# Optimization experiments

Measured on AMD Instinct MI355X. Metric: run time of the kernel, lower is better.

Reference implementation:

```python
import jax, jax.numpy as jnp
import numpy as np

NEG = -1e30


def setup_inputs() -> dict:
    key = jax.random.key(0)
    ks = jax.random.split(key, 8)
    B, d, Lc, Lq = 32, 128, 2048, 512
    C = jax.random.normal(ks[0], (B, d, Lc), dtype=jnp.float32)
    Q = jax.random.normal(ks[1], (B, d, Lq), dtype=jnp.float32)
    Cmask = jax.random.randint(ks[2], (B, Lc), 0, 2, dtype=jnp.int32)
    Qmask = jax.random.randint(ks[3], (B, Lq), 0, 2, dtype=jnp.int32)
    # xavier_uniform over (d, 1): bound = sqrt(6 / (d + 1))
    bnd = float(np.sqrt(6.0 / (d + 1)))
    w_c = jax.random.uniform(ks[4], (d, 1), minval=-bnd, maxval=bnd, dtype=jnp.float32)
    w_q = jax.random.uniform(ks[5], (d, 1), minval=-bnd, maxval=bnd, dtype=jnp.float32)
    bnd_m = float(np.sqrt(6.0 / (1 + d)))
    w_mul = jax.random.uniform(ks[6], (1, 1, d), minval=-bnd_m, maxval=bnd_m, dtype=jnp.float32)
    bias = jnp.zeros((1,), dtype=jnp.float32)
    return {"C": C, "Q": Q, "Cmask": Cmask, "Qmask": Qmask,
            "w_c": w_c, "w_q": w_q, "w_mul": w_mul, "bias": bias}


def reference(C, Q, Cmask, Qmask, w_c, w_q, w_mul, bias):
    # C: [B, d, Lc], Q: [B, d, Lq] -> transpose to token-major
    Ct = jnp.swapaxes(C, 1, 2)  # [B, Lc, d]
    Qt = jnp.swapaxes(Q, 1, 2)  # [B, Lq, d]
    cm = Cmask.astype(jnp.float32)[:, :, None]   # [B, Lc, 1]
    qm = Qmask.astype(jnp.float32)[:, None, :]   # [B, 1, Lq]
    # optimized trilinear similarity S: [B, Lc, Lq] (dropout p=0 / eval mode)
    s0 = Ct @ w_c                                  # [B, Lc, 1]
    s1 = jnp.swapaxes(Qt @ w_q, 1, 2)              # [B, 1, Lq]
    s2 = jnp.einsum('bcd,bqd->bcq', Ct * w_mul, Qt)  # [B, Lc, Lq]
    S = s0 + s1 + s2 + bias
    S1 = jax.nn.softmax(S + NEG * (1.0 - qm), axis=2)  # mask over query axis
    S2 = jax.nn.softmax(S + NEG * (1.0 - cm), axis=1)  # mask over context axis
    A = jnp.einsum('bcq,bqd->bcd', S1, Qt)             # [B, Lc, d]
    Bm = jnp.einsum('bck,bkd->bcd', jnp.einsum('bcq,bkq->bck', S1, S2), Ct)
    out = jnp.concatenate([Ct, A, Ct * A, Ct * Bm], axis=2)  # [B, Lc, 4d]
    return jnp.swapaxes(out, 1, 2)  # [B, 4d, Lc]
```

## Files before the change

kernel.cpp:

```cpp
#include <hip/hip_runtime.h>

#define B_ 32
#define D_ 128
#define LC 2048
#define LQ 512
#define CCH 16

#define NEGINF (-3.0e38f)

typedef __attribute__((ext_vector_type(8))) short bf16x8;
typedef __attribute__((ext_vector_type(4))) float f32x4;
typedef __attribute__((ext_vector_type(8))) unsigned short us8;
typedef __attribute__((ext_vector_type(8))) _Float16 f16x8;

__device__ __forceinline__ unsigned short bf16rne(float x) {
    unsigned int u = __float_as_uint(x);
    u = (u + 0x7FFFu + ((u >> 16) & 1u)) >> 16;
    return (unsigned short)u;
}

__device__ __forceinline__ void gll16(const void* g, void* l) {
    __builtin_amdgcn_global_load_lds((const __attribute__((address_space(1))) void*)g,
                                     (__attribute__((address_space(3))) void*)l, 16, 0, 0);
}

__global__ void k_dotw(const float* __restrict__ X, const float* __restrict__ w,
                       float* __restrict__ outv, int L) {
    int idx = blockIdx.x * 256 + threadIdx.x;
    int b = idx / L, x = idx - b * L;
    const float* Xp = X + (size_t)b * D_ * L + x;
    float acc = 0.f;
#pragma unroll 8
    for (int dd = 0; dd < D_; ++dd) acc += Xp[(size_t)dd * L] * w[dd];
    outv[idx] = acc;
}

__global__ void k_prep_C(const float* __restrict__ C, const float* __restrict__ wmul,
                         short* __restrict__ Ctw, short* __restrict__ Cb16) {
    int b = blockIdx.y, c0 = blockIdx.x * 64;
    __shared__ float Tf[128][65];
    __shared__ float wm[128];
    int t = threadIdx.x;
    if (t < 128) wm[t] = wmul[t];
    const float* Cb = C + (size_t)b * D_ * LC;
#pragma unroll
    for (int i = 0; i < 8; ++i) {
        int idx = t + i * 256;
        int d = idx >> 4, c4 = idx & 15;
        float4 v = *(const float4*)(Cb + (size_t)d * LC + c0 + c4 * 4);
        Tf[d][c4 * 4 + 0] = v.x; Tf[d][c4 * 4 + 1] = v.y;
        Tf[d][c4 * 4 + 2] = v.z; Tf[d][c4 * 4 + 3] = v.w;
        ushort4 cv;
        cv.x = bf16rne(v.x); cv.y = bf16rne(v.y); cv.z = bf16rne(v.z); cv.w = bf16rne(v.w);
        *(ushort4*)(Cb16 + ((size_t)b * D_ + d) * LC + c0 + c4 * 4) = cv;
    }
    __syncthreads();
    int c_l = t & 63, g = t >> 6;
    unsigned short u[32];
#pragma unroll
    for (int j = 0; j < 32; ++j) {
        int d = g * 32 + j;
        u[j] = bf16rne(Tf[d][c_l] * wm[d]);
    }
    short* dst = Ctw + ((size_t)b * LC + c0 + c_l) * D_ + g * 32;
#pragma unroll
    for (int k = 0; k < 4; ++k) *(us8*)(dst + k * 8) = *(const us8*)&u[k * 8];
}

__global__ void k_prep_Q(const float* __restrict__ Q, short* __restrict__ Qt16,
                         short* __restrict__ Wf) {
    int b = blockIdx.y, q0 = blockIdx.x * 64;
    __shared__ float Tf[128][65];
    int t = threadIdx.x;
    const float* Qb = Q + (size_t)b * D_ * LQ;
#pragma unroll
    for (int i = 0; i < 8; ++i) {
        int idx = t + i * 256;
        int d = idx >> 4, q4 = idx & 15;
        float4 v = *(const float4*)(Qb + (size_t)d * LQ + q0 + q4 * 4);
        Tf[d][q4 * 4 + 0] = v.x; Tf[d][q4 * 4 + 1] = v.y;
        Tf[d][q4 * 4 + 2] = v.z; Tf[d][q4 * 4 + 3] = v.w;
        ushort4 cv;
        cv.x = bf16rne(v.x); cv.y = bf16rne(v.y); cv.z = bf16rne(v.z); cv.w = bf16rne(v.w);
        *(ushort4*)(Wf + ((size_t)b * 256 + d) * LQ + q0 + q4 * 4) = cv;
    }
    __syncthreads();
    int q_l = t & 63, g = t >> 6;
    unsigned short u[32];
#pragma unroll
    for (int j = 0; j < 32; ++j) u[j] = bf16rne(Tf[g * 32 + j][q_l]);
    short* dst = Qt16 + ((size_t)b * LQ + q0 + q_l) * D_ + g * 32;
#pragma unroll
    for (int k = 0; k < 4; ++k) *(us8*)(dst + k * 8) = *(const us8*)&u[k * 8];
}

__global__ __launch_bounds__(256) void k_S_mfma(const short* __restrict__ Ctw,
                                                const short* __restrict__ Qt16,
                                                const float* __restrict__ s0,
                                                const float* __restrict__ s1,
                                                const float* __restrict__ bias,
                                                const int* __restrict__ Cmask,
                                                _Float16* __restrict__ S16,
                                                float* __restrict__ pm,
                                                float* __restrict__ pl) {
    int b = blockIdx.y;
    int cT = blockIdx.x >> 2, qT = blockIdx.x & 3;
    int c0 = cT * 128, q0 = qT * 128;
    int t = threadIdx.x, w = t >> 6, l = t & 63;
    int wm_ = w >> 1, wn = w & 1;
    __shared__ short As[128 * 64];
    __shared__ short Bs[128 * 64];
    f32x4 acc[4][4] = {};
    const short* Arow = Ctw + ((size_t)b * LC + c0) * D_;
    const short* Brow = Qt16 + ((size_t)b * LQ + q0) * D_;
    int lr = l >> 3, sl = l & 7;
    for (int kt = 0; kt < 2; ++kt) {
        __syncthreads();
#pragma unroll
        for (int i = 0; i < 4; ++i) {
            int r = w * 32 + i * 8 + lr;
            int g = sl ^ (r & 7);
            gll16(Arow + (size_t)r * D_ + kt * 64 + g * 8, &As[(w * 32 + i * 8) * 64]);
            gll16(Brow + (size_t)r * D_ + kt * 64 + g * 8, &Bs[(w * 32 + i * 8) * 64]);
        }
        __syncthreads();
#pragma unroll
        for (int ks = 0; ks < 2; ++ks) {
            int kg = ks * 4 + (l >> 4);
            bf16x8 af[4], bfr[4];
#pragma unroll
            for (int ms = 0; ms < 4; ++ms) {
                int m = wm_ * 64 + ms * 16 + (l & 15);
                af[ms] = *(const bf16x8*)&As[m * 64 + (kg ^ (m & 7)) * 8];
            }
#pragma unroll
            for (int ns = 0; ns < 4; ++ns) {
                int n = wn * 64 + ns * 16 + (l & 15);
                bfr[ns] = *(const bf16x8*)&Bs[n * 64 + (kg ^ (n & 7)) * 8];
            }
#pragma unroll
            for (int ms = 0; ms < 4; ++ms)
#pragma unroll
                for (int ns = 0; ns < 4; ++ns)
                    acc[ms][ns] = __builtin_amdgcn_mfma_f32_16x16x32_bf16(af[ms], bfr[ns], acc[ms][ns], 0, 0, 0);
        }
    }
    float bv = bias[0];
    float s0v[16];
    int cmv[16];
#pragma unroll
    for (int ms = 0; ms < 4; ++ms) {
        int cb = c0 + wm_ * 64 + ms * 16 + (l >> 4) * 4;
        float4 sv = *(const float4*)(s0 + b * LC + cb);
        s0v[ms * 4 + 0] = sv.x; s0v[ms * 4 + 1] = sv.y;
        s0v[ms * 4 + 2] = sv.z; s0v[ms * 4 + 3] = sv.w;
        int4 cv = *(const int4*)(Cmask + b * LC + cb);
        cmv[ms * 4 + 0] = cv.x; cmv[ms * 4 + 1] = cv.y;
        cmv[ms * 4 + 2] = cv.z; cmv[ms * 4 + 3] = cv.w;
    }
    __syncthreads();
    float* Mp = (float*)As;
    float* Lp = (float*)Bs;
    int prow = wm_ * 4 + (l >> 4);
#pragma unroll
    for (int ns = 0; ns < 4; ++ns) {
        int qi = wn * 64 + ns * 16 + (l & 15);
        int q = q0 + qi;
        float s1v = s1[b * LQ + q] + bv;
        float vq16[16];
#pragma unroll
        for (int ms = 0; ms < 4; ++ms) {
            int cb = c0 + wm_ * 64 + ms * 16 + (l >> 4) * 4;
#pragma unroll
            for (int r = 0; r < 4; ++r) {
                float vf = acc[ms][ns][r] + s0v[ms * 4 + r] + s1v;
                _Float16 h = (_Float16)vf;
                S16[((size_t)b * LC + cb + r) * LQ + q] = h;
                vq16[ms * 4 + r] = (float)h;
            }
        }
        float mt = NEGINF;
#pragma unroll
        for (int k = 0; k < 16; ++k) mt = fmaxf(mt, cmv[k] ? vq16[k] : NEGINF);
        float st = 0.f;
#pragma unroll
        for (int k = 0; k < 16; ++k) st += cmv[k] ? __expf(vq16[k] - mt) : 0.f;
        Mp[prow * 132 + qi] = mt;
        Lp[prow * 132 + qi] = st;
    }
    __syncthreads();
    if (t < 128) {
        float mm = Mp[t], ll = Lp[t];
#pragma unroll
        for (int g = 1; g < 8; ++g) {
            float m2 = Mp[g * 132 + t], l2 = Lp[g * 132 + t];
            float mn = fmaxf(mm, m2);
            ll = ll * __expf(mm - mn) + l2 * __expf(m2 - mn);
            mm = mn;
        }
        size_t o = ((size_t)cT * B_ + b) * LQ + q0 + t;
        pm[o] = mm; pl[o] = ll;
    }
}

__global__ void k_rowstats(const _Float16* __restrict__ S16, const int* __restrict__ Qmask,
                           float* __restrict__ rowmax, float* __restrict__ rowsum) {
    int row = blockIdx.x * 4 + (threadIdx.x >> 6);
    int lane = threadIdx.x & 63;
    int b = row / LC;
    f16x8 v = *(const f16x8*)(S16 + (size_t)row * LQ + lane * 8);
    const int* qm = Qmask + b * LQ + lane * 8;
    int4 m0 = *(const int4*)qm;
    int4 m1 = *(const int4*)(qm + 4);
    int mk[8] = {m0.x, m0.y, m0.z, m0.w, m1.x, m1.y, m1.z, m1.w};
    float vf[8];
#pragma unroll
    for (int k = 0; k < 8; ++k) vf[k] = (float)v[k];
    float mx = NEGINF;
#pragma unroll
    for (int k = 0; k < 8; ++k) if (mk[k]) mx = fmaxf(mx, vf[k]);
#pragma unroll
    for (int off = 32; off > 0; off >>= 1) mx = fmaxf(mx, __shfl_xor(mx, off, 64));
    float s = 0.f;
#pragma unroll
    for (int k = 0; k < 8; ++k) if (mk[k]) s += __expf(vf[k] - mx);
#pragma unroll
    for (int off = 32; off > 0; off >>= 1) s += __shfl_xor(s, off, 64);
    if (lane == 0) { rowmax[row] = mx; rowsum[row] = s; }
}

__global__ void k_colstats_comb(const float* __restrict__ pm, const float* __restrict__ pl,
                                float* __restrict__ colmax, float* __restrict__ colsum) {
    int idx = blockIdx.x * 256 + threadIdx.x;
    float m = NEGINF, l = 0.f;
#pragma unroll
    for (int ch = 0; ch < CCH; ++ch) {
        float m2 = pm[(size_t)ch * B_ * LQ + idx];
        float l2 = pl[(size_t)ch * B_ * LQ + idx];
        float mn = fmaxf(m, m2);
        l = l * __expf(m - mn) + l2 * __expf(m2 - mn);
        m = mn;
    }
    colmax[idx] = m; colsum[idx] = l;
}

__global__ __launch_bounds__(256) void k_V2_mfma(const short* __restrict__ Cb16,
                                                 _Float16* __restrict__ S16,
                                                 const int* __restrict__ Cmask,
                                                 const int* __restrict__ Qmask,
                                                 const float* __restrict__ colmax,
                                                 const float* __restrict__ colsum,
                                                 const float* __restrict__ rowmax,
                                                 const float* __restrict__ rowsum,
                                                 short* __restrict__ Wf) {
    int b = blockIdx.y;
    int q0 = blockIdx.x * 64;
    int t = threadIdx.x, w = t >> 6, l = t & 63;
    __shared__ short As[128 * 64];
    __shared__ short Bs[64 * 72];
    f32x4 acc[2][4] = {};
    const short* Arow = Cb16 + (size_t)b * D_ * LC;
    int lr = l >> 3, sl = l & 7;
    float cmx[16];
#pragma unroll
    for (int j2 = 0; j2 < 4; ++j2)
        *(float4*)&cmx[j2 * 4] = *(const float4*)(colmax + b * LQ + q0 + w * 16 + j2 * 4);
    int qmv[16];
#pragma unroll
    for (int j2 = 0; j2 < 4; ++j2)
        *(int4*)&qmv[j2 * 4] = *(const int4*)(Qmask + b * LQ + q0 + w * 16 + j2 * 4);
    _Float16* Sq = S16 + (size_t)b * LC * LQ + q0 + w * 16;
    const int* cmb = Cmask + b * LC;
    const float* rmb = rowmax + b * LC;
    const float* rsb = rowsum + b * LC;

    for (int kt = 0; kt < 32; ++kt) {
        int ck = kt * 64;
        __syncthreads();
#pragma unroll
        for (int i = 0; i < 4; ++i) {
            int r = w * 32 + i * 8 + lr;
            int g = sl ^ (r & 7);
            gll16(Arow + (size_t)r * LC + ck + g * 8, &As[(w * 32 + i * 8) * 64]);
        }
        {
            int c = ck + l;
            float cmf = (float)cmb[c];
            float rm = rmb[c];
            float ri = 1.0f / rsb[c];
            _Float16* sp = Sq + (size_t)c * LQ;
            f16x8 v0 = *(const f16x8*)sp;
            f16x8 v1 = *(const f16x8*)(sp + 8);
#pragma unroll
            for (int j = 0; j < 8; ++j)
                Bs[(w * 16 + j) * 72 + l] = (short)bf16rne(cmf * __expf((float)v0[j] - cmx[j]));
#pragma unroll
            for (int j = 0; j < 8; ++j)
                Bs[(w * 16 + 8 + j) * 72 + l] = (short)bf16rne(cmf * __expf((float)v1[j] - cmx[8 + j]));
            unsigned short p0[8], p1r[8];
#pragma unroll
            for (int j = 0; j < 8; ++j)
                p0[j] = qmv[j] ? bf16rne(__expf((float)v0[j] - rm) * ri) : (unsigned short)0;
#pragma unroll
            for (int j = 0; j < 8; ++j)
                p1r[j] = qmv[8 + j] ? bf16rne(__expf((float)v1[j] - rm) * ri) : (unsigned short)0;
            *(us8*)sp = *(const us8*)&p0[0];
            *(us8*)(sp + 8) = *(const us8*)&p1r[0];
        }
        __syncthreads();
#pragma unroll
        for (int ks = 0; ks < 2; ++ks) {
            int kg = ks * 4 + (l >> 4);
            bf16x8 af[2], bfr[4];
#pragma unroll
            for (int ms = 0; ms < 2; ++ms) {
                int m = w * 32 + ms * 16 + (l & 15);
                af[ms] = *(const bf16x8*)&As[m * 64 + (kg ^ (m & 7)) * 8];
            }
#pragma unroll
            for (int ns = 0; ns < 4; ++ns) {
                int n = ns * 16 + (l & 15);
                bfr[ns] = *(const bf16x8*)&Bs[n * 72 + kg * 8];
            }
#pragma unroll
            for (int ms = 0; ms < 2; ++ms)
#pragma unroll
                for (int ns = 0; ns < 4; ++ns)
                    acc[ms][ns] = __builtin_amdgcn_mfma_f32_16x16x32_bf16(af[ms], bfr[ns], acc[ms][ns], 0, 0, 0);
        }
    }
#pragma unroll
    for (int ms = 0; ms < 2; ++ms)
#pragma unroll
        for (int ns = 0; ns < 4; ++ns) {
            int q = q0 + ns * 16 + (l & 15);
            float csi = 1.0f / colsum[b * LQ + q];
#pragma unroll
            for (int r = 0; r < 4; ++r) {
                int dd = w * 32 + ms * 16 + (l >> 4) * 4 + r;
                Wf[((size_t)b * 256 + 128 + dd) * LQ + q] = (short)bf16rne(acc[ms][ns][r] * csi);
            }
        }
}

__global__ __launch_bounds__(512) void k_out_mfma(const short* __restrict__ P1,
                                                  const short* __restrict__ Wf,
                                                  const float* __restrict__ C,
                                                  float* __restrict__ out) {
    int b = blockIdx.y;
    int c0 = blockIdx.x * 128;
    int t = threadIdx.x, w = t >> 6, l = t & 63;
    int wn = w & 3, wc = w >> 2;
    __shared__ short As[2 * 256 * 64];
    __shared__ short Bs[128 * 64];
    f32x4 acc[4][4] = {};
    const short* Arow = Wf + (size_t)b * 256 * LQ;
    const short* Brow = P1 + ((size_t)b * LC + c0) * LQ;
    int lr = l >> 3, sl = l & 7;
    int g = sl ^ lr;

#define STAGE_A(p, kt)                                                            \
    {                                                                             \
        short* Ad = As + (p) * (256 * 64);                                        \
        _Pragma("unroll")                                                         \
        for (int i = 0; i < 4; ++i) {                                             \
            int r = w * 32 + i * 8 + lr;                                          \
            gll16(Arow + (size_t)r * LQ + (kt) * 64 + g * 8,                      \
                  &Ad[(w * 32 + i * 8) * 64]);                                    \
        }                                                                         \
    }
#define STAGE_B(kt)                                                               \
    {                                                                             \
        _Pragma("unroll")                                                         \
        for (int i = 0; i < 2; ++i) {                                             \
            int r = w * 16 + i * 8 + lr;                                          \
            gll16(Brow + (size_t)r * LQ + (kt) * 64 + g * 8,                      \
                  &Bs[(w * 16 + i * 8) * 64]);                                    \
        }                                                                         \
    }

    STAGE_B(0);
    STAGE_A(0, 0);
    STAGE_A(1, 1);
    int cur = 0;
    for (int kt = 0; kt < 8; ++kt) {
        if (kt < 7) asm volatile("s_waitcnt vmcnt(4)" ::: "memory");
        else        asm volatile("s_waitcnt vmcnt(0)" ::: "memory");
        __builtin_amdgcn_s_barrier();
        __builtin_amdgcn_sched_barrier(0);
        const short* Ac = As + cur * (256 * 64);
#pragma unroll
        for (int ks = 0; ks < 2; ++ks) {
            int kg = ks * 4 + (l >> 4);
            bf16x8 af[4], bfr[4];
#pragma unroll
            for (int ms = 0; ms < 4; ++ms) {
                int m = wn * 64 + ms * 16 + (l & 15);
                af[ms] = *(const bf16x8*)&Ac[m * 64 + (kg ^ (m & 7)) * 8];
            }
#pragma unroll
            for (int ns = 0; ns < 4; ++ns) {
                int cc = wc * 64 + ns * 16 + (l & 15);
                bfr[ns] = *(const bf16x8*)&Bs[cc * 64 + (kg ^ (cc & 7)) * 8];
            }
#pragma unroll
            for (int ms = 0; ms < 4; ++ms)
#pragma unroll
                for (int ns = 0; ns < 4; ++ns)
                    acc[ms][ns] = __builtin_amdgcn_mfma_f32_16x16x32_bf16(af[ms], bfr[ns], acc[ms][ns], 0, 0, 0);
        }
        __builtin_amdgcn_s_barrier();
        __builtin_amdgcn_sched_barrier(0);
        if (kt < 7) {
            STAGE_B(kt + 1);
            if (kt < 6) STAGE_A(cur, kt + 2);
        }
        cur ^= 1;
    }
#undef STAGE_A
#undef STAGE_B
#pragma unroll
    for (int ms = 0; ms < 4; ++ms) {
        int nb = wn * 64 + ms * 16 + (l >> 4) * 4;
#pragma unroll
        for (int ns = 0; ns < 4; ++ns) {
            int c = c0 + wc * 64 + ns * 16 + (l & 15);
#pragma unroll
            for (int r = 0; r < 4; ++r) {
                int n = nb + r;
                float a = acc[ms][ns][r];
                if (n < 128) {
                    float cv = C[((size_t)b * D_ + n) * LC + c];
                    out[((size_t)b * 512 + n) * LC + c] = cv;
                    out[((size_t)b * 512 + 128 + n) * LC + c] = a;
                    out[((size_t)b * 512 + 256 + n) * LC + c] = cv * a;
                } else {
                    int dd = n - 128;
                    float cv = C[((size_t)b * D_ + dd) * LC + c];
                    out[((size_t)b * 512 + 384 + dd) * LC + c] = cv * a;
                }
            }
        }
    }
}

extern "C" void kernel_launch(void* const* d_in, const int* in_sizes, int n_in,
                              void* d_out, int out_size, void* d_ws, size_t ws_size,
                              hipStream_t stream) {
    const float* C     = (const float*)d_in[0];
    const float* Q     = (const float*)d_in[1];
    const int*   Cmask = (const int*)d_in[2];
    const int*   Qmask = (const int*)d_in[3];
    const float* w_c   = (const float*)d_in[4];
    const float* w_q   = (const float*)d_in[5];
    const float* w_mul = (const float*)d_in[6];
    const float* bias  = (const float*)d_in[7];
    float* out = (float*)d_out;

    _Float16* S16 = (_Float16*)d_ws;
    short* Cb16 = (short*)(S16 + (size_t)B_ * LC * LQ);
    short* Ctw  = Cb16 + (size_t)B_ * D_ * LC;
    short* Qt16 = Ctw + (size_t)B_ * LC * D_;
    short* Wf   = Qt16 + (size_t)B_ * LQ * D_;
    float* s0     = (float*)(Wf + (size_t)B_ * 256 * LQ);
    float* s1     = s0 + B_ * LC;
    float* colmax = s1 + B_ * LQ;
    float* colsum = colmax + B_ * LQ;
    float* rowmax = colsum + B_ * LQ;
    float* rowsum = rowmax + B_ * LC;
    float* pm     = rowsum + B_ * LC;
    float* pl     = pm + (size_t)CCH * B_ * LQ;

    hipLaunchKernelGGL(k_dotw, dim3(B_ * LC / 256), dim3(256), 0, stream, C, w_c, s0, LC);
    hipLaunchKernelGGL(k_dotw, dim3(B_ * LQ / 256), dim3(256), 0, stream, Q, w_q, s1, LQ);
    hipLaunchKernelGGL(k_prep_C, dim3(LC / 64, B_), dim3(256), 0, stream, C, w_mul, Ctw, Cb16);
    hipLaunchKernelGGL(k_prep_Q, dim3(LQ / 64, B_), dim3(256), 0, stream, Q, Qt16, Wf);
    hipLaunchKernelGGL(k_S_mfma, dim3((LC / 128) * (LQ / 128), B_), dim3(256), 0, stream,
                       Ctw, Qt16, s0, s1, bias, Cmask, S16, pm, pl);
    hipLaunchKernelGGL(k_colstats_comb, dim3(B_ * LQ / 256), dim3(256), 0, stream,
                       pm, pl, colmax, colsum);
    hipLaunchKernelGGL(k_rowstats, dim3(B_ * LC / 4), dim3(256), 0, stream, S16, Qmask, rowmax, rowsum);
    hipLaunchKernelGGL(k_V2_mfma, dim3(LQ / 64, B_), dim3(256), 0, stream,
                       Cb16, S16, Cmask, Qmask, colmax, colsum, rowmax, rowsum, Wf);
    hipLaunchKernelGGL(k_out_mfma, dim3(LC / 128, B_), dim3(512), 0, stream,
                       (const short*)S16, Wf, C, out);
}
```

Measured before the change: 397.3 us.

## Fuse row softmax stats into S kernel, merge combines, double-buffer out GEMM

Computes per-row online max/sum partials inside the S GEMM epilogue, so the separate rowstats kernel no longer has to re-read the full fp16 S matrix. Row and column partials are then merged in a single combine kernel. It also replaces __syncthreads with raw barriers plus explicit waitcnt in the V2 kernel, and switches the output GEMM to a uniform double-buffered A/B prefetch. The cost is extra exp work and shuffle reductions in the S epilogue, and more LDS in the output kernel.

```diff
diff --git a/kernel.cpp b/kernel.cpp
--- a/kernel.cpp
+++ b/kernel.cpp
@@ -5,6 +5,7 @@
 #define LC 2048
 #define LQ 512
 #define CCH 16
+#define RCH 4
 
 #define NEGINF (-3.0e38f)
 
@@ -100,9 +101,12 @@
                                                 const float* __restrict__ s1,
                                                 const float* __restrict__ bias,
                                                 const int* __restrict__ Cmask,
+                                                const int* __restrict__ Qmask,
                                                 _Float16* __restrict__ S16,
                                                 float* __restrict__ pm,
-                                                float* __restrict__ pl) {
+                                                float* __restrict__ pl,
+                                                float* __restrict__ pmr,
+                                                float* __restrict__ plr) {
     int b = blockIdx.y;
     int cT = blockIdx.x >> 2, qT = blockIdx.x & 3;
     int c0 = cT * 128, q0 = qT * 128;
@@ -158,15 +162,21 @@
         cmv[ms * 4 + 0] = cv.x; cmv[ms * 4 + 1] = cv.y;
         cmv[ms * 4 + 2] = cv.z; cmv[ms * 4 + 3] = cv.w;
     }
+    float rm_[16], rs_[16];
+#pragma unroll
+    for (int k = 0; k < 16; ++k) { rm_[k] = NEGINF; rs_[k] = 0.f; }
     __syncthreads();
     float* Mp = (float*)As;
     float* Lp = (float*)Bs;
+    float* Rmf = (float*)As + 2048;
+    float* Rsf = (float*)Bs + 2048;
     int prow = wm_ * 4 + (l >> 4);
 #pragma unroll
     for (int ns = 0; ns < 4; ++ns) {
         int qi = wn * 64 + ns * 16 + (l & 15);
         int q = q0 + qi;
         float s1v = s1[b * LQ + q] + bv;
+        int qmn = Qmask[b * LQ + q];
         float vq16[16];
 #pragma unroll
         for (int ms = 0; ms < 4; ++ms) {
@@ -187,6 +197,34 @@
         for (int k = 0; k < 16; ++k) st += cmv[k] ? __expf(vq16[k] - mt) : 0.f;
         Mp[prow * 132 + qi] = mt;
         Lp[prow * 132 + qi] = st;
+#pragma unroll
+        for (int k = 0; k < 16; ++k) {
+            float v = qmn ? vq16[k] : NEGINF;
+            float mn = fmaxf(rm_[k], v);
+            rs_[k] = rs_[k] * __expf(rm_[k] - mn) + __expf(v - mn);
+            rm_[k] = mn;
+        }
+    }
+#pragma unroll
+    for (int off = 1; off < 16; off <<= 1) {
+#pragma unroll
+        for (int k = 0; k < 16; ++k) {
+            float m2 = __shfl_xor(rm_[k], off, 64);
+            float l2 = __shfl_xor(rs_[k], off, 64);
+            float mn = fmaxf(rm_[k], m2);
+            rs_[k] = rs_[k] * __expf(rm_[k] - mn) + l2 * __expf(m2 - mn);
+            rm_[k] = mn;
+        }
+    }
+    if ((l & 15) == 0) {
+#pragma unroll
+        for (int ms = 0; ms < 4; ++ms)
+#pragma unroll
+            for (int r = 0; r < 4; ++r) {
+                int cl = wm_ * 64 + ms * 16 + (l >> 4) * 4 + r;
+                Rmf[wn * 128 + cl] = rm_[ms * 4 + r];
+                Rsf[wn * 128 + cl] = rs_[ms * 4 + r];
+            }
     }
     __syncthreads();
     if (t < 128) {
@@ -200,48 +238,47 @@
         }
         size_t o = ((size_t)cT * B_ + b) * LQ + q0 + t;
         pm[o] = mm; pl[o] = ll;
-    }
-}
-
-__global__ void k_rowstats(const _Float16* __restrict__ S16, const int* __restrict__ Qmask,
-                           float* __restrict__ rowmax, float* __restrict__ rowsum) {
-    int row = blockIdx.x * 4 + (threadIdx.x >> 6);
-    int lane = threadIdx.x & 63;
-    int b = row / LC;
-    f16x8 v = *(const f16x8*)(S16 + (size_t)row * LQ + lane * 8);
-    const int* qm = Qmask + b * LQ + lane * 8;
-    int4 m0 = *(const int4*)qm;
-    int4 m1 = *(const int4*)(qm + 4);
-    int mk[8] = {m0.x, m0.y, m0.z, m0.w, m1.x, m1.y, m1.z, m1.w};
-    float vf[8];
-#pragma unroll
-    for (int k = 0; k < 8; ++k) vf[k] = (float)v[k];
-    float mx = NEGINF;
-#pragma unroll
-    for (int k = 0; k < 8; ++k) if (mk[k]) mx = fmaxf(mx, vf[k]);
-#pragma unroll
-    for (int off = 32; off > 0; off >>= 1) mx = fmaxf(mx, __shfl_xor(mx, off, 64));
-    float s = 0.f;
-#pragma unroll
-    for (int k = 0; k < 8; ++k) if (mk[k]) s += __expf(vf[k] - mx);
-#pragma unroll
-    for (int off = 32; off > 0; off >>= 1) s += __shfl_xor(s, off, 64);
-    if (lane == 0) { rowmax[row] = mx; rowsum[row] = s; }
-}
-
-__global__ void k_colstats_comb(const float* __restrict__ pm, const float* __restrict__ pl,
-                                float* __restrict__ colmax, float* __restrict__ colsum) {
-    int idx = blockIdx.x * 256 + threadIdx.x;
-    float m = NEGINF, l = 0.f;
-#pragma unroll
-    for (int ch = 0; ch < CCH; ++ch) {
-        float m2 = pm[(size_t)ch * B_ * LQ + idx];
-        float l2 = pl[(size_t)ch * B_ * LQ + idx];
-        float mn = fmaxf(m, m2);
-        l = l * __expf(m - mn) + l2 * __expf(m2 - mn);
-        m = mn;
-    }
-    colmax[idx] = m; colsum[idx] = l;
+        float rm0 = Rmf[t], rs0 = Rsf[t];
+        float rm1 = Rmf[128 + t], rs1 = Rsf[128 + t];
+        if (rm0 == NEGINF) rs0 = 0.f;
+        if (rm1 == NEGINF) rs1 = 0.f;
+        float mn = fmaxf(rm0, rm1);
+        float lo = rs0 * __expf(rm0 - mn) + rs1 * __expf(rm1 - mn);
+        size_t orow = ((size_t)qT * B_ + b) * LC + c0 + t;
+        pmr[orow] = mn; plr[orow] = lo;
+    }
+}
+
+__global__ void k_comb(const float* __restrict__ pm, const float* __restrict__ pl,
+                       const float* __restrict__ pmr, const float* __restrict__ plr,
+                       float* __restrict__ colmax, float* __restrict__ colsum,
+                       float* __restrict__ rowmax, float* __restrict__ rowsum) {
+    int bx = blockIdx.x;
+    if (bx < (B_ * LQ) / 256) {
+        int idx = bx * 256 + threadIdx.x;
+        float m = NEGINF, l = 0.f;
+#pragma unroll
+        for (int ch = 0; ch < CCH; ++ch) {
+            float m2 = pm[(size_t)ch * B_ * LQ + idx];
+            float l2 = pl[(size_t)ch * B_ * LQ + idx];
+            float mn = fmaxf(m, m2);
+            l = l * __expf(m - mn) + l2 * __expf(m2 - mn);
+            m = mn;
+        }
+        colmax[idx] = m; colsum[idx] = l;
+    } else {
+        int idx = (bx - (B_ * LQ) / 256) * 256 + threadIdx.x;
+        float m = NEGINF, l = 0.f;
+#pragma unroll
+        for (int ch = 0; ch < RCH; ++ch) {
+            float m2 = pmr[(size_t)ch * B_ * LC + idx];
+            float l2 = plr[(size_t)ch * B_ * LC + idx];
+            float mn = fmaxf(m, m2);
+            l = l * __expf(m - mn) + l2 * __expf(m2 - mn);
+            m = mn;
+        }
+        rowmax[idx] = m; rowsum[idx] = l;
+    }
 }
 
 __global__ __launch_bounds__(256) void k_V2_mfma(const short* __restrict__ Cb16,
@@ -276,7 +313,8 @@
 
     for (int kt = 0; kt < 32; ++kt) {
         int ck = kt * 64;
-        __syncthreads();
+        __builtin_amdgcn_s_barrier();
+        __builtin_amdgcn_sched_barrier(0);
 #pragma unroll
         for (int i = 0; i < 4; ++i) {
             int r = w * 32 + i * 8 + lr;
@@ -304,10 +342,13 @@
 #pragma unroll
             for (int j = 0; j < 8; ++j)
                 p1r[j] = qmv[8 + j] ? bf16rne(__expf((float)v1[j] - rm) * ri) : (unsigned short)0;
+            __builtin_amdgcn_sched_barrier(0);
             *(us8*)sp = *(const us8*)&p0[0];
             *(us8*)(sp + 8) = *(const us8*)&p1r[0];
         }
-        __syncthreads();
+        asm volatile("s_waitcnt vmcnt(2) lgkmcnt(0)" ::: "memory");
+        __builtin_amdgcn_s_barrier();
+        __builtin_amdgcn_sched_barrier(0);
 #pragma unroll
         for (int ks = 0; ks < 2; ++ks) {
             int kg = ks * 4 + (l >> 4);
@@ -352,43 +393,44 @@
     int t = threadIdx.x, w = t >> 6, l = t & 63;
     int wn = w & 3, wc = w >> 2;
     __shared__ short As[2 * 256 * 64];
-    __shared__ short Bs[128 * 64];
+    __shared__ short Bs[2 * 128 * 64];
     f32x4 acc[4][4] = {};
     const short* Arow = Wf + (size_t)b * 256 * LQ;
     const short* Brow = P1 + ((size_t)b * LC + c0) * LQ;
     int lr = l >> 3, sl = l & 7;
     int g = sl ^ lr;
 
-#define STAGE_A(p, kt)                                                            \
+#define STAGE(p, kt)                                                              \
     {                                                                             \
         short* Ad = As + (p) * (256 * 64);                                        \
+        short* Bd = Bs + (p) * (128 * 64);                                        \
         _Pragma("unroll")                                                         \
         for (int i = 0; i < 4; ++i) {                                             \
             int r = w * 32 + i * 8 + lr;                                          \
             gll16(Arow + (size_t)r * LQ + (kt) * 64 + g * 8,                      \
                   &Ad[(w * 32 + i * 8) * 64]);                                    \
         }                                                                         \
-    }
-#define STAGE_B(kt)                                                               \
-    {                                                                             \
         _Pragma("unroll")                                                         \
         for (int i = 0; i < 2; ++i) {                                             \
             int r = w * 16 + i * 8 + lr;                                          \
             gll16(Brow + (size_t)r * LQ + (kt) * 64 + g * 8,                      \
-                  &Bs[(w * 16 + i * 8) * 64]);                                    \
+                  &Bd[(w * 16 + i * 8) * 64]);                                    \
         }                                                                         \
     }
 
-    STAGE_B(0);
-    STAGE_A(0, 0);
-    STAGE_A(1, 1);
+    STAGE(0, 0);
     int cur = 0;
     for (int kt = 0; kt < 8; ++kt) {
-        if (kt < 7) asm volatile("s_waitcnt vmcnt(4)" ::: "memory");
-        else        asm volatile("s_waitcnt vmcnt(0)" ::: "memory");
+        if (kt < 7) {
+            STAGE(cur ^ 1, kt + 1);
+            asm volatile("s_waitcnt vmcnt(6)" ::: "memory");
+        } else {
+            asm volatile("s_waitcnt vmcnt(0)" ::: "memory");
+        }
         __builtin_amdgcn_s_barrier();
         __builtin_amdgcn_sched_barrier(0);
         const short* Ac = As + cur * (256 * 64);
+        const short* Bc = Bs + cur * (128 * 64);
 #pragma unroll
         for (int ks = 0; ks < 2; ++ks) {
             int kg = ks * 4 + (l >> 4);
@@ -401,7 +443,7 @@
 #pragma unroll
             for (int ns = 0; ns < 4; ++ns) {
                 int cc = wc * 64 + ns * 16 + (l & 15);
-                bfr[ns] = *(const bf16x8*)&Bs[cc * 64 + (kg ^ (cc & 7)) * 8];
+                bfr[ns] = *(const bf16x8*)&Bc[cc * 64 + (kg ^ (cc & 7)) * 8];
             }
 #pragma unroll
             for (int ms = 0; ms < 4; ++ms)
@@ -410,15 +452,9 @@
                     acc[ms][ns] = __builtin_amdgcn_mfma_f32_16x16x32_bf16(af[ms], bfr[ns], acc[ms][ns], 0, 0, 0);
         }
         __builtin_amdgcn_s_barrier();
-        __builtin_amdgcn_sched_barrier(0);
-        if (kt < 7) {
-            STAGE_B(kt + 1);
-            if (kt < 6) STAGE_A(cur, kt + 2);
-        }
         cur ^= 1;
     }
-#undef STAGE_A
-#undef STAGE_B
+#undef STAGE
 #pragma unroll
     for (int ms = 0; ms < 4; ++ms) {
         int nb = wn * 64 + ms * 16 + (l >> 4) * 4;
@@ -470,16 +506,17 @@
     float* rowsum = rowmax + B_ * LC;
     float* pm     = rowsum + B_ * LC;
     float* pl     = pm + (size_t)CCH * B_ * LQ;
+    float* pmr    = pl + (size_t)CCH * B_ * LQ;
+    float* plr    = pmr + (size_t)RCH * B_ * LC;
 
     hipLaunchKernelGGL(k_dotw, dim3(B_ * LC / 256), dim3(256), 0, stream, C, w_c, s0, LC);
     hipLaunchKernelGGL(k_dotw, dim3(B_ * LQ / 256), dim3(256), 0, stream, Q, w_q, s1, LQ);
     hipLaunchKernelGGL(k_prep_C, dim3(LC / 64, B_), dim3(256), 0, stream, C, w_mul, Ctw, Cb16);
     hipLaunchKernelGGL(k_prep_Q, dim3(LQ / 64, B_), dim3(256), 0, stream, Q, Qt16, Wf);
     hipLaunchKernelGGL(k_S_mfma, dim3((LC / 128) * (LQ / 128), B_), dim3(256), 0, stream,
-                       Ctw, Qt16, s0, s1, bias, Cmask, S16, pm, pl);
-    hipLaunchKernelGGL(k_colstats_comb, dim3(B_ * LQ / 256), dim3(256), 0, stream,
-                       pm, pl, colmax, colsum);
-    hipLaunchKernelGGL(k_rowstats, dim3(B_ * LC / 4), dim3(256), 0, stream, S16, Qmask, rowmax, rowsum);
+                       Ctw, Qt16, s0, s1, bias, Cmask, Qmask, S16, pm, pl, pmr, plr);
+    hipLaunchKernelGGL(k_comb, dim3((B_ * LQ + B_ * LC) / 256), dim3(256), 0, stream,
+                       pm, pl, pmr, plr, colmax, colsum, rowmax, rowsum);
     hipLaunchKernelGGL(k_V2_mfma, dim3(LQ / 64, B_), dim3(256), 0, stream,
                        Cb16, S16, Cmask, Qmask, colmax, colsum, rowmax, rowsum, Wf);
     hipLaunchKernelGGL(k_out_mfma, dim3(LC / 128, B_), dim3(512), 0, stream,
```

Measured after the change: 422.7 us. 1.06x slower.
